# Performance work log

Hardware: AMD Instinct MI355X
Metric: run time of the kernel (lower is better)

Reference implementation:

```python
import jax, jax.numpy as jnp
import numpy as np

DIMS = [2048, 2048, 2048, 2048, 1000]
BATCH = 1024
N_RELAX = 25
RELAX_LR = 0.3
N_LAYERS = len(DIMS) - 1  # 4 weight matrices, states indexed 0..4


def setup_inputs() -> dict:
    key = jax.random.key(0)
    ks = jax.random.split(key, N_LAYERS + 1)
    inp = {"x": jax.random.normal(ks[0], (BATCH, DIMS[0]), jnp.float32)}
    for i in range(N_LAYERS):
        scale = np.float32(np.sqrt(2.0 / DIMS[i]))
        inp[f"W{i}"] = jax.random.normal(ks[i + 1], (DIMS[i], DIMS[i + 1]), jnp.float32) * scale
    # biases[0] is never used in forward; biases[1..4] init to zeros as in torch code
    for l in range(1, N_LAYERS + 1):
        inp[f"b{l}"] = jnp.zeros((DIMS[l],), jnp.float32)
    return inp


def _rho(t):
    return jnp.clip(t, 0.0, 1.0)


def _relax(x, Ws, bs):
    # bs[l-1] corresponds to original biases[l] (state l's bias), l = 1..N_LAYERS
    # feedforward initialization pass
    states = [x]
    h = x
    for l in range(N_LAYERS):
        h = _rho(h @ Ws[l] + bs[l])
        states.append(h)

    # Gauss-Seidel sweep: states[l-1] already updated this iteration when l uses it
    def sweep(carry, _):
        full = [x] + list(carry)
        for l in range(1, N_LAYERS + 1):
            ds = -full[l] + bs[l - 1] + _rho(full[l - 1]) @ Ws[l - 1]
            if l < N_LAYERS:
                ds = ds + _rho(full[l + 1]) @ Ws[l].T
            full[l] = _rho(full[l] + RELAX_LR * ds)
        return tuple(full[1:]), None

    carry, _ = jax.lax.scan(sweep, tuple(states[1:]), None, length=N_RELAX)
    return carry


def reference(x, W0, W1, W2, W3, b1, b2, b3, b4):
    Ws = [W0, W1, W2, W3]
    bs = [b1, b2, b3, b4]
    states = _relax(x, Ws, bs)
    return states[-1]  # [BATCH, DIMS[-1]]
```

## Files before the change

kernel.cpp:

```cpp
#include <hip/hip_runtime.h>
#include <hip/hip_bf16.h>

typedef _Float16 fp16_t;
typedef _Float16 v8h __attribute__((ext_vector_type(8)));
typedef float    v4f __attribute__((ext_vector_type(4)));

#define RELAX_LR 0.3f

__device__ __forceinline__ void async_cp16(const void* g, void* l) {
    __builtin_amdgcn_global_load_lds(
        (const __attribute__((address_space(1))) void*)g,
        (__attribute__((address_space(3))) void*)l, 16, 0, 0);
}

struct GJob {
    const fp16_t *A1, *B1t, *A2, *B2t;
    fp16_t* part;
    int K1, K2s, CK, Ntot;
};

__global__ __launch_bounds__(256, 2) void gemm_splitk_kernel(GJob j0, GJob j1, int nb0)
{
    __shared__ __align__(16) fp16_t As[2][2][128][32];
    __shared__ __align__(16) fp16_t Bs[2][2][128][32];

    const int tid  = threadIdx.x;
    const int lane = tid & 63;
    const int w    = tid >> 6;
    const int wm   = w >> 1;
    const int wn   = w & 1;
    const int quad = lane >> 4;
    const int lrow = lane & 15;

    int bblk = blockIdx.x;
    const GJob j = (bblk < nb0) ? j0 : j1;
    if (bblk >= nb0) bblk -= nb0;

    const int low3 = bblk & 7;
    const int g    = bblk >> 3;
    const int bm   = g & 7;
    const int c    = (g >> 3) * 8 + low3;
    int bn, z;
    if (j.Ntot == 2048) { bn = c >> 2; z = c & 3; }
    else                { bn = c >> 3; z = c & 7; }
    const int k0 = z * j.CK;

    const int sr = lane >> 2;
    const int sc = (lane & 3) * 8;
    const size_t rowA = (size_t)(bm * 128 + 32 * w + sr);
    const size_t rowB = (size_t)(bn * 128 + 32 * w + sr);
    const fp16_t* a1 = j.A1  + rowA * j.K1 + sc;
    const fp16_t* b1 = j.B1t + rowB * j.K1 + sc;
    const fp16_t* a2 = j.A2  ? j.A2  + rowA * j.K2s + sc : nullptr;
    const fp16_t* b2 = j.B2t ? j.B2t + rowB * j.K2s + sc : nullptr;
    const size_t s16a = (size_t)16 * j.K1;
    const size_t s16b = (size_t)16 * j.K2s;

    auto stage = [&](int buf, int kc) {
        const fp16_t *a0, *b0; size_t st;
        if (kc < j.K1) { a0 = a1 + kc;          b0 = b1 + kc;          st = s16a; }
        else           { a0 = a2 + (kc - j.K1); b0 = b2 + (kc - j.K1); st = s16b; }
        async_cp16(a0,           &As[buf][0][32 * w     ][0]);
        async_cp16(a0 + st,      &As[buf][0][32 * w + 16][0]);
        async_cp16(a0 + 32,      &As[buf][1][32 * w     ][0]);
        async_cp16(a0 + 32 + st, &As[buf][1][32 * w + 16][0]);
        async_cp16(b0,           &Bs[buf][0][32 * w     ][0]);
        async_cp16(b0 + st,      &Bs[buf][0][32 * w + 16][0]);
        async_cp16(b0 + 32,      &Bs[buf][1][32 * w     ][0]);
        async_cp16(b0 + 32 + st, &Bs[buf][1][32 * w + 16][0]);
    };

    v4f acc[4][4] = {};
    const int iters = j.CK >> 6;

    stage(0, k0);

    for (int it = 0; it < iters; ++it) {
        __syncthreads();
        if (it + 1 < iters) stage((it + 1) & 1, k0 + (it + 1) * 64);
        const int cur = it & 1;
        #pragma unroll
        for (int h = 0; h < 2; ++h) {
            v8h af[4], bv[4];
            #pragma unroll
            for (int fm = 0; fm < 4; ++fm)
                af[fm] = *(const v8h*)&As[cur][h][wm * 64 + fm * 16 + lrow][quad * 8];
            #pragma unroll
            for (int fn = 0; fn < 4; ++fn)
                bv[fn] = *(const v8h*)&Bs[cur][h][wn * 64 + fn * 16 + lrow][quad * 8];
            #pragma unroll
            for (int fm = 0; fm < 4; ++fm)
                #pragma unroll
                for (int fn = 0; fn < 4; ++fn)
                    acc[fm][fn] = __builtin_amdgcn_mfma_f32_16x16x32_f16(
                        af[fm], bv[fn], acc[fm][fn], 0, 0, 0);
        }
    }

    fp16_t* po = j.part + (size_t)z * 1024 * j.Ntot;
    const int rowbase = bm * 128 + wm * 64 + quad * 4;
    const int colbase = bn * 128 + wn * 64;
    #pragma unroll
    for (int fn = 0; fn < 4; ++fn) {
        const int col = colbase + fn * 16 + lrow;
        #pragma unroll
        for (int fm = 0; fm < 4; ++fm) {
            const int row = rowbase + fm * 16;
            #pragma unroll
            for (int r = 0; r < 4; ++r)
                po[(size_t)(row + r) * j.Ntot + col] = (fp16_t)acc[fm][fn][r];
        }
    }
}

struct RJob {
    const fp16_t* part;
    const float* bias;
    const float* extra;
    const fp16_t* s_old;
    fp16_t* outb;
    float* finout;
    int nz, Ntot, do_update;
};

__global__ __launch_bounds__(256) void reduce_update_kernel(RJob j0, RJob j1, int nb0)
{
    int b = blockIdx.x;
    const RJob j = (b < nb0) ? j0 : j1;
    if (b >= nb0) b -= nb0;
    const size_t e = ((size_t)b * 256 + threadIdx.x) * 8;

    float v[8];
    {
        const v8h p0 = *(const v8h*)(j.part + e);
        #pragma unroll
        for (int k = 0; k < 8; ++k) v[k] = (float)p0[k];
    }
    for (int z = 1; z < j.nz; ++z) {
        const v8h p = *(const v8h*)(j.part + (size_t)z * 1024 * j.Ntot + e);
        #pragma unroll
        for (int k = 0; k < 8; ++k) v[k] += (float)p[k];
    }
    const int col = (int)e & (j.Ntot - 1);
    if (j.extra) {
        const float4 e0 = *(const float4*)(j.extra + e);
        const float4 e1 = *(const float4*)(j.extra + e + 4);
        v[0] += e0.x; v[1] += e0.y; v[2] += e0.z; v[3] += e0.w;
        v[4] += e1.x; v[5] += e1.y; v[6] += e1.z; v[7] += e1.w;
    } else {
        const float4 b0 = *(const float4*)(j.bias + col);
        const float4 b1 = *(const float4*)(j.bias + col + 4);
        v[0] += b0.x; v[1] += b0.y; v[2] += b0.z; v[3] += b0.w;
        v[4] += b1.x; v[5] += b1.y; v[6] += b1.z; v[7] += b1.w;
    }
    if (j.do_update) {
        const v8h so = *(const v8h*)(j.s_old + e);
        #pragma unroll
        for (int k = 0; k < 8; ++k) {
            const float s = (float)so[k];
            v[k] = s + RELAX_LR * (v[k] - s);
        }
    }
    #pragma unroll
    for (int k = 0; k < 8; ++k) v[k] = fminf(fmaxf(v[k], 0.f), 1.f);
    v8h h;
    #pragma unroll
    for (int k = 0; k < 8; ++k) h[k] = (fp16_t)v[k];
    *(v8h*)(j.outb + e) = h;

    if (j.finout && col < 1000) {
        const int row = (int)(e >> 10);
        float* o = j.finout + (size_t)row * 1000 + col;
        float4 o0 = {v[0], v[1], v[2], v[3]};
        float4 o1 = {v[4], v[5], v[6], v[7]};
        *(float4*)o       = o0;
        *(float4*)(o + 4) = o1;
    }
}

__global__ __launch_bounds__(256) void makec1_kernel(
    const fp16_t* __restrict__ part, const float* __restrict__ bias,
    float* __restrict__ c1f, int total8)
{
    const int i = blockIdx.x * 256 + threadIdx.x;
    if (i >= total8) return;
    const size_t e = (size_t)i * 8;
    float v[8];
    {
        const v8h p0 = *(const v8h*)(part + e);
        #pragma unroll
        for (int k = 0; k < 8; ++k) v[k] = (float)p0[k];
    }
    #pragma unroll
    for (int z = 1; z < 4; ++z) {
        const v8h p = *(const v8h*)(part + (size_t)z * 1024 * 2048 + e);
        #pragma unroll
        for (int k = 0; k < 8; ++k) v[k] += (float)p[k];
    }
    const int col = (int)e & 2047;
    const float4 b0 = *(const float4*)(bias + col);
    const float4 b1 = *(const float4*)(bias + col + 4);
    v[0] += b0.x; v[1] += b0.y; v[2] += b0.z; v[3] += b0.w;
    v[4] += b1.x; v[5] += b1.y; v[6] += b1.z; v[7] += b1.w;
    float4 o0 = {v[0], v[1], v[2], v[3]};
    float4 o1 = {v[4], v[5], v[6], v[7]};
    *(float4*)(c1f + e)     = o0;
    *(float4*)(c1f + e + 4) = o1;
}

__global__ void conv_w_kernel(const float* __restrict__ W, int R, int C,
                              fp16_t* Wb, fp16_t* __restrict__ WbT,
                              int Rp, int Cp)
{
    __shared__ float t[32][33];
    const int tx = threadIdx.x & 31;
    const int ty = threadIdx.x >> 5;
    const int r0 = blockIdx.y * 32;
    const int c0 = blockIdx.x * 32;
    #pragma unroll
    for (int i = 0; i < 4; ++i) {
        const int r = r0 + ty + i * 8;
        const int c = c0 + tx;
        float v = 0.f;
        if (r < R && c < C) v = W[(size_t)r * C + c];
        t[ty + i * 8][tx] = v;
    }
    __syncthreads();
    if (Wb) {
        #pragma unroll
        for (int i = 0; i < 4; ++i) {
            const int r = r0 + ty + i * 8;
            const int c = c0 + tx;
            if (r < Rp && c < Cp) Wb[(size_t)r * Cp + c] = (fp16_t)t[ty + i * 8][tx];
        }
    }
    #pragma unroll
    for (int i = 0; i < 4; ++i) {
        const int cc = c0 + ty + i * 8;
        const int rr = r0 + tx;
        if (cc < Cp && rr < Rp) WbT[(size_t)cc * Rp + rr] = (fp16_t)t[tx][ty + i * 8];
    }
}

__global__ void conv_x_kernel(const float* __restrict__ x,
                              fp16_t* __restrict__ xb, fp16_t* __restrict__ rxb, int n)
{
    const int i = blockIdx.x * blockDim.x + threadIdx.x;
    if (i < n) {
        const float v = x[i];
        xb[i]  = (fp16_t)v;
        rxb[i] = (fp16_t)fminf(fmaxf(v, 0.f), 1.f);
    }
}

__global__ void pad_b4_kernel(const float* __restrict__ b4, float* __restrict__ b4p)
{
    const int i = blockIdx.x * blockDim.x + threadIdx.x;
    if (i < 1024) b4p[i] = (i < 1000) ? b4[i] : 0.f;
}

extern "C" void kernel_launch(void* const* d_in, const int* in_sizes, int n_in,
                              void* d_out, int out_size, void* d_ws, size_t ws_size,
                              hipStream_t stream)
{
    const float* x  = (const float*)d_in[0];
    const float* W0 = (const float*)d_in[1];
    const float* W1 = (const float*)d_in[2];
    const float* W2 = (const float*)d_in[3];
    const float* W3 = (const float*)d_in[4];
    const float* b1 = (const float*)d_in[5];
    const float* b2 = (const float*)d_in[6];
    const float* b3 = (const float*)d_in[7];
    const float* b4 = (const float*)d_in[8];
    float* out = (float*)d_out;

    char* p = (char*)d_ws;
    auto alloc = [&](size_t bytes) {
        char* q = p;
        p += (bytes + 255) & ~(size_t)255;
        return q;
    };

    fp16_t* xb    = (fp16_t*)alloc((size_t)1024 * 2048 * 2);
    fp16_t* rxb   = (fp16_t*)alloc((size_t)1024 * 2048 * 2);
    fp16_t* Wb1   = (fp16_t*)alloc((size_t)2048 * 2048 * 2);
    fp16_t* Wb2   = (fp16_t*)alloc((size_t)2048 * 2048 * 2);
    fp16_t* Wb3   = (fp16_t*)alloc((size_t)2048 * 1024 * 2);
    fp16_t* WbT0  = (fp16_t*)alloc((size_t)2048 * 2048 * 2);
    fp16_t* WbT1  = (fp16_t*)alloc((size_t)2048 * 2048 * 2);
    fp16_t* WbT2  = (fp16_t*)alloc((size_t)2048 * 2048 * 2);
    fp16_t* WbT3  = (fp16_t*)alloc((size_t)1024 * 2048 * 2);
    fp16_t* s1b   = (fp16_t*)alloc((size_t)1024 * 2048 * 2);
    fp16_t* s2b   = (fp16_t*)alloc((size_t)1024 * 2048 * 2);
    fp16_t* s3b   = (fp16_t*)alloc((size_t)1024 * 2048 * 2);
    fp16_t* s4b   = (fp16_t*)alloc((size_t)1024 * 1024 * 2);
    float*  b4p   = (float*)alloc(1024 * 4);
    float*  c1f   = (float*)alloc((size_t)1024 * 2048 * 4);
    fp16_t* partA = (fp16_t*)alloc((size_t)8 * 1024 * 1024 * 2);
    fp16_t* partB = (fp16_t*)alloc((size_t)4 * 1024 * 2048 * 2);
    (void)ws_size; (void)in_sizes; (void)n_in; (void)out_size;

    conv_x_kernel<<<(1024 * 2048 + 255) / 256, 256, 0, stream>>>(x, xb, rxb, 1024 * 2048);
    pad_b4_kernel<<<4, 256, 0, stream>>>(b4, b4p);
    conv_w_kernel<<<dim3(64, 64), 256, 0, stream>>>(W0, 2048, 2048, nullptr, WbT0, 2048, 2048);
    conv_w_kernel<<<dim3(64, 64), 256, 0, stream>>>(W1, 2048, 2048, Wb1, WbT1, 2048, 2048);
    conv_w_kernel<<<dim3(64, 64), 256, 0, stream>>>(W2, 2048, 2048, Wb2, WbT2, 2048, 2048);
    conv_w_kernel<<<dim3(32, 64), 256, 0, stream>>>(W3, 2048, 1000, Wb3, WbT3, 2048, 1024);

    const dim3 blk(256);
    const int rg2048 = 1024 * 2048 / 8 / 256;
    const int rg1024 = 1024 * 1024 / 8 / 256;

    const GJob jC1 = { rxb, WbT0, nullptr, nullptr, partA, 2048, 0,    512,  2048 };
    const GJob jI1 = { xb,  WbT0, nullptr, nullptr, partB, 2048, 0,    512,  2048 };
    const GJob jI2 = { s1b, WbT1, nullptr, nullptr, partB, 2048, 0,    512,  2048 };
    const GJob jI3 = { s2b, WbT2, nullptr, nullptr, partB, 2048, 0,    512,  2048 };
    const GJob jI4 = { s3b, WbT3, nullptr, nullptr, partA, 2048, 0,    256,  1024 };
    const GJob jL1 = { s2b, Wb1,  nullptr, nullptr, partB, 2048, 0,    512,  2048 };
    const GJob jL2 = { s1b, WbT1, s3b, Wb2,         partB, 2048, 2048, 1024, 2048 };
    const GJob jL3 = { s2b, WbT2, s4b, Wb3,         partB, 2048, 1024, 768,  2048 };
    const GJob jL4 = { s3b, WbT3, nullptr, nullptr, partA, 2048, 0,    256,  1024 };

    const RJob rI1 = { partB, b1,  nullptr, nullptr, s1b, nullptr, 4, 2048, 0 };
    const RJob rI2 = { partB, b2,  nullptr, nullptr, s2b, nullptr, 4, 2048, 0 };
    const RJob rI3 = { partB, b3,  nullptr, nullptr, s3b, nullptr, 4, 2048, 0 };
    const RJob rI4 = { partA, b4p, nullptr, nullptr, s4b, nullptr, 8, 1024, 0 };
    const RJob rL1 = { partB, nullptr, c1f, s1b, s1b, nullptr, 4, 2048, 1 };
    const RJob rL2 = { partB, b2,  nullptr, s2b, s2b, nullptr, 4, 2048, 1 };
    const RJob rL3 = { partB, b3,  nullptr, s3b, s3b, nullptr, 4, 2048, 1 };
    const RJob rL4 = { partA, b4p, nullptr, s4b, s4b, nullptr, 8, 1024, 1 };
    RJob rL4f = rL4; rL4f.finout = out;

    gemm_splitk_kernel<<<512, blk, 0, stream>>>(jC1, jC1, 512);
    makec1_kernel<<<rg2048, blk, 0, stream>>>(partA, b1, c1f, 1024 * 2048 / 8);

    gemm_splitk_kernel<<<512, blk, 0, stream>>>(jI1, jI1, 512);
    reduce_update_kernel<<<rg2048, blk, 0, stream>>>(rI1, rI1, rg2048);
    gemm_splitk_kernel<<<512, blk, 0, stream>>>(jI2, jI2, 512);
    reduce_update_kernel<<<rg2048, blk, 0, stream>>>(rI2, rI2, rg2048);
    gemm_splitk_kernel<<<512, blk, 0, stream>>>(jI3, jI3, 512);
    reduce_update_kernel<<<rg2048, blk, 0, stream>>>(rI3, rI3, rg2048);
    gemm_splitk_kernel<<<512, blk, 0, stream>>>(jI4, jI4, 512);
    reduce_update_kernel<<<rg1024, blk, 0, stream>>>(rI4, rI4, rg1024);

    gemm_splitk_kernel<<<512, blk, 0, stream>>>(jL1, jL1, 512);
    reduce_update_kernel<<<rg2048, blk, 0, stream>>>(rL1, rL1, rg2048);
    for (int it = 0; it < 25; ++it) {
        gemm_splitk_kernel<<<512, blk, 0, stream>>>(jL2, jL2, 512);
        reduce_update_kernel<<<rg2048, blk, 0, stream>>>(rL2, rL2, rg2048);
        gemm_splitk_kernel<<<512, blk, 0, stream>>>(jL3, jL3, 512);
        reduce_update_kernel<<<rg2048, blk, 0, stream>>>(rL3, rL3, rg2048);
        if (it < 24) {
            gemm_splitk_kernel<<<1024, blk, 0, stream>>>(jL4, jL1, 512);
            reduce_update_kernel<<<rg1024 + rg2048, blk, 0, stream>>>(rL4, rL1, rg1024);
        } else {
            gemm_splitk_kernel<<<512, blk, 0, stream>>>(jL4, jL4, 512);
            reduce_update_kernel<<<rg1024, blk, 0, stream>>>(rL4f, rL4f, rg1024);
        }
    }
}
```

Before: 2.411 ms.

## Fuse split-K reduction and state update into GEMM via intra-block K split

Replaces the global split-K GEMM plus separate reduce/update kernels with one fused kernel. Each block computes a 64x64 output tile, its four waves take disjoint K quarters with per-wave LDS double buffering, and the partials are reduced through LDS. Bias, extra term, relaxation update, clamp and the fp16/fp32 stores then happen in the epilogue. This removes the fp16 partial-sum round trips through global memory and halves kernel launches. In exchange the tiles are smaller, per-wave loads are synchronised with manual waitcnt, and the epilogue writes are scalar per element.

Result: slower. 3.226 ms (+33.8%).

```diff
diff --git a/kernel.cpp b/kernel.cpp
--- a/kernel.cpp
+++ b/kernel.cpp
@@ -1,5 +1,4 @@
 #include <hip/hip_runtime.h>
-#include <hip/hip_bf16.h>
 
 typedef _Float16 fp16_t;
 typedef _Float16 v8h __attribute__((ext_vector_type(8)));
@@ -13,199 +12,126 @@
         (__attribute__((address_space(3))) void*)l, 16, 0, 0);
 }
 
-struct GJob {
+struct FJob {
     const fp16_t *A1, *B1t, *A2, *B2t;
-    fp16_t* part;
-    int K1, K2s, CK, Ntot;
+    const float  *bias;
+    const float  *extra;
+    const fp16_t *s_old;
+    fp16_t       *outb;
+    float        *f32out;
+    float        *finout;
+    int K1, K2s, Ktot, Ntot;
 };
 
-__global__ __launch_bounds__(256, 2) void gemm_splitk_kernel(GJob j0, GJob j1, int nb0)
-{
-    __shared__ __align__(16) fp16_t As[2][2][128][32];
-    __shared__ __align__(16) fp16_t Bs[2][2][128][32];
+__global__ __launch_bounds__(256, 2) void gemm_fused_kernel(FJob j0, FJob j1, int nb0)
+{
+    __shared__ __align__(16) fp16_t sm[4][2][2][64][32];
 
     const int tid  = threadIdx.x;
     const int lane = tid & 63;
     const int w    = tid >> 6;
-    const int wm   = w >> 1;
-    const int wn   = w & 1;
     const int quad = lane >> 4;
     const int lrow = lane & 15;
 
     int bblk = blockIdx.x;
-    const GJob j = (bblk < nb0) ? j0 : j1;
+    const FJob j = (bblk < nb0) ? j0 : j1;
     if (bblk >= nb0) bblk -= nb0;
 
-    const int low3 = bblk & 7;
-    const int g    = bblk >> 3;
-    const int bm   = g & 7;
-    const int c    = (g >> 3) * 8 + low3;
-    int bn, z;
-    if (j.Ntot == 2048) { bn = c >> 2; z = c & 3; }
-    else                { bn = c >> 3; z = c & 7; }
-    const int k0 = z * j.CK;
-
-    const int sr = lane >> 2;
-    const int sc = (lane & 3) * 8;
-    const size_t rowA = (size_t)(bm * 128 + 32 * w + sr);
-    const size_t rowB = (size_t)(bn * 128 + 32 * w + sr);
-    const fp16_t* a1 = j.A1  + rowA * j.K1 + sc;
-    const fp16_t* b1 = j.B1t + rowB * j.K1 + sc;
-    const fp16_t* a2 = j.A2  ? j.A2  + rowA * j.K2s + sc : nullptr;
-    const fp16_t* b2 = j.B2t ? j.B2t + rowB * j.K2s + sc : nullptr;
-    const size_t s16a = (size_t)16 * j.K1;
-    const size_t s16b = (size_t)16 * j.K2s;
+    const int xcd = bblk & 7;
+    const int g   = bblk >> 3;
+    const int bm  = g & 15;
+    const int bn  = (j.Ntot == 2048) ? xcd * 4 + (g >> 4)
+                                     : xcd * 2 + (g >> 4);
+
+    const int KQ  = j.Ktot >> 2;
+    const int kq0 = w * KQ;
+
+    const int sr  = lane >> 2;
+    const int sc8 = (lane & 3) * 8;
+    const fp16_t* a1 = j.A1  + (size_t)(bm * 64 + sr) * j.K1 + sc8;
+    const fp16_t* b1 = j.B1t + (size_t)(bn * 64 + sr) * j.K1 + sc8;
+    const fp16_t* a2 = j.A2  ? j.A2  + (size_t)(bm * 64 + sr) * j.K2s + sc8 : nullptr;
+    const fp16_t* b2 = j.B2t ? j.B2t + (size_t)(bn * 64 + sr) * j.K2s + sc8 : nullptr;
 
     auto stage = [&](int buf, int kc) {
-        const fp16_t *a0, *b0; size_t st;
-        if (kc < j.K1) { a0 = a1 + kc;          b0 = b1 + kc;          st = s16a; }
-        else           { a0 = a2 + (kc - j.K1); b0 = b2 + (kc - j.K1); st = s16b; }
-        async_cp16(a0,           &As[buf][0][32 * w     ][0]);
-        async_cp16(a0 + st,      &As[buf][0][32 * w + 16][0]);
-        async_cp16(a0 + 32,      &As[buf][1][32 * w     ][0]);
-        async_cp16(a0 + 32 + st, &As[buf][1][32 * w + 16][0]);
-        async_cp16(b0,           &Bs[buf][0][32 * w     ][0]);
-        async_cp16(b0 + st,      &Bs[buf][0][32 * w + 16][0]);
-        async_cp16(b0 + 32,      &Bs[buf][1][32 * w     ][0]);
-        async_cp16(b0 + 32 + st, &Bs[buf][1][32 * w + 16][0]);
+        const fp16_t *as, *bs; size_t st;
+        if (kc < j.K1) { as = a1 + kc;          bs = b1 + kc;          st = (size_t)16 * j.K1;  }
+        else           { as = a2 + (kc - j.K1); bs = b2 + (kc - j.K1); st = (size_t)16 * j.K2s; }
+        #pragma unroll
+        for (int ch = 0; ch < 4; ++ch) {
+            async_cp16(as + (size_t)ch * st, &sm[w][buf][0][ch * 16][0]);
+            async_cp16(bs + (size_t)ch * st, &sm[w][buf][1][ch * 16][0]);
+        }
     };
 
     v4f acc[4][4] = {};
-    const int iters = j.CK >> 6;
-
-    stage(0, k0);
-
+    const int iters = KQ >> 5;
+
+    stage(0, kq0);
     for (int it = 0; it < iters; ++it) {
-        __syncthreads();
-        if (it + 1 < iters) stage((it + 1) & 1, k0 + (it + 1) * 64);
         const int cur = it & 1;
-        #pragma unroll
-        for (int h = 0; h < 2; ++h) {
-            v8h af[4], bv[4];
-            #pragma unroll
-            for (int fm = 0; fm < 4; ++fm)
-                af[fm] = *(const v8h*)&As[cur][h][wm * 64 + fm * 16 + lrow][quad * 8];
+        if (it + 1 < iters) {
+            asm volatile("s_waitcnt lgkmcnt(0)" ::: "memory");
+            stage(cur ^ 1, kq0 + (it + 1) * 32);
+            asm volatile("s_waitcnt vmcnt(8)" ::: "memory");
+        } else {
+            asm volatile("s_waitcnt vmcnt(0)" ::: "memory");
+        }
+        v8h af[4], bv[4];
+        #pragma unroll
+        for (int fm = 0; fm < 4; ++fm)
+            af[fm] = *(const v8h*)&sm[w][cur][0][fm * 16 + lrow][quad * 8];
+        #pragma unroll
+        for (int fn = 0; fn < 4; ++fn)
+            bv[fn] = *(const v8h*)&sm[w][cur][1][fn * 16 + lrow][quad * 8];
+        __builtin_amdgcn_s_setprio(1);
+        #pragma unroll
+        for (int fm = 0; fm < 4; ++fm)
             #pragma unroll
             for (int fn = 0; fn < 4; ++fn)
-                bv[fn] = *(const v8h*)&Bs[cur][h][wn * 64 + fn * 16 + lrow][quad * 8];
-            #pragma unroll
-            for (int fm = 0; fm < 4; ++fm)
-                #pragma unroll
-                for (int fn = 0; fn < 4; ++fn)
-                    acc[fm][fn] = __builtin_amdgcn_mfma_f32_16x16x32_f16(
-                        af[fm], bv[fn], acc[fm][fn], 0, 0, 0);
-        }
-    }
-
-    fp16_t* po = j.part + (size_t)z * 1024 * j.Ntot;
-    const int rowbase = bm * 128 + wm * 64 + quad * 4;
-    const int colbase = bn * 128 + wn * 64;
-    #pragma unroll
-    for (int fn = 0; fn < 4; ++fn) {
-        const int col = colbase + fn * 16 + lrow;
-        #pragma unroll
-        for (int fm = 0; fm < 4; ++fm) {
-            const int row = rowbase + fm * 16;
+                acc[fm][fn] = __builtin_amdgcn_mfma_f32_16x16x32_f16(
+                    af[fm], bv[fn], acc[fm][fn], 0, 0, 0);
+        __builtin_amdgcn_s_setprio(0);
+    }
+
+    __syncthreads();
+    float* red = (float*)sm;
+    #pragma unroll
+    for (int fm = 0; fm < 4; ++fm)
+        #pragma unroll
+        for (int fn = 0; fn < 4; ++fn)
             #pragma unroll
             for (int r = 0; r < 4; ++r)
-                po[(size_t)(row + r) * j.Ntot + col] = (fp16_t)acc[fm][fn][r];
-        }
-    }
-}
-
-struct RJob {
-    const fp16_t* part;
-    const float* bias;
-    const float* extra;
-    const fp16_t* s_old;
-    fp16_t* outb;
-    float* finout;
-    int nz, Ntot, do_update;
-};
-
-__global__ __launch_bounds__(256) void reduce_update_kernel(RJob j0, RJob j1, int nb0)
-{
-    int b = blockIdx.x;
-    const RJob j = (b < nb0) ? j0 : j1;
-    if (b >= nb0) b -= nb0;
-    const size_t e = ((size_t)b * 256 + threadIdx.x) * 8;
-
-    float v[8];
-    {
-        const v8h p0 = *(const v8h*)(j.part + e);
-        #pragma unroll
-        for (int k = 0; k < 8; ++k) v[k] = (float)p0[k];
-    }
-    for (int z = 1; z < j.nz; ++z) {
-        const v8h p = *(const v8h*)(j.part + (size_t)z * 1024 * j.Ntot + e);
-        #pragma unroll
-        for (int k = 0; k < 8; ++k) v[k] += (float)p[k];
-    }
-    const int col = (int)e & (j.Ntot - 1);
-    if (j.extra) {
-        const float4 e0 = *(const float4*)(j.extra + e);
-        const float4 e1 = *(const float4*)(j.extra + e + 4);
-        v[0] += e0.x; v[1] += e0.y; v[2] += e0.z; v[3] += e0.w;
-        v[4] += e1.x; v[5] += e1.y; v[6] += e1.z; v[7] += e1.w;
-    } else {
-        const float4 b0 = *(const float4*)(j.bias + col);
-        const float4 b1 = *(const float4*)(j.bias + col + 4);
-        v[0] += b0.x; v[1] += b0.y; v[2] += b0.z; v[3] += b0.w;
-        v[4] += b1.x; v[5] += b1.y; v[6] += b1.z; v[7] += b1.w;
-    }
-    if (j.do_update) {
-        const v8h so = *(const v8h*)(j.s_old + e);
-        #pragma unroll
-        for (int k = 0; k < 8; ++k) {
-            const float s = (float)so[k];
-            v[k] = s + RELAX_LR * (v[k] - s);
-        }
-    }
-    #pragma unroll
-    for (int k = 0; k < 8; ++k) v[k] = fminf(fmaxf(v[k], 0.f), 1.f);
-    v8h h;
-    #pragma unroll
-    for (int k = 0; k < 8; ++k) h[k] = (fp16_t)v[k];
-    *(v8h*)(j.outb + e) = h;
-
-    if (j.finout && col < 1000) {
-        const int row = (int)(e >> 10);
-        float* o = j.finout + (size_t)row * 1000 + col;
-        float4 o0 = {v[0], v[1], v[2], v[3]};
-        float4 o1 = {v[4], v[5], v[6], v[7]};
-        *(float4*)o       = o0;
-        *(float4*)(o + 4) = o1;
-    }
-}
-
-__global__ __launch_bounds__(256) void makec1_kernel(
-    const fp16_t* __restrict__ part, const float* __restrict__ bias,
-    float* __restrict__ c1f, int total8)
-{
-    const int i = blockIdx.x * 256 + threadIdx.x;
-    if (i >= total8) return;
-    const size_t e = (size_t)i * 8;
-    float v[8];
-    {
-        const v8h p0 = *(const v8h*)(part + e);
-        #pragma unroll
-        for (int k = 0; k < 8; ++k) v[k] = (float)p0[k];
-    }
-    #pragma unroll
-    for (int z = 1; z < 4; ++z) {
-        const v8h p = *(const v8h*)(part + (size_t)z * 1024 * 2048 + e);
-        #pragma unroll
-        for (int k = 0; k < 8; ++k) v[k] += (float)p[k];
-    }
-    const int col = (int)e & 2047;
-    const float4 b0 = *(const float4*)(bias + col);
-    const float4 b1 = *(const float4*)(bias + col + 4);
-    v[0] += b0.x; v[1] += b0.y; v[2] += b0.z; v[3] += b0.w;
-    v[4] += b1.x; v[5] += b1.y; v[6] += b1.z; v[7] += b1.w;
-    float4 o0 = {v[0], v[1], v[2], v[3]};
-    float4 o1 = {v[4], v[5], v[6], v[7]};
-    *(float4*)(c1f + e)     = o0;
-    *(float4*)(c1f + e + 4) = o1;
+                red[((w * 64 + fm * 16 + fn * 4 + r) << 6) + lane] = acc[fm][fn][r];
+    __syncthreads();
+
+    const int rowbase = bm * 64 + w * 16 + quad * 4;
+    const int colbase = bn * 64;
+    #pragma unroll
+    for (int u = 0; u < 16; ++u) {
+        const int s = w * 16 + u;
+        float v = red[( s        << 6) + lane]
+                + red[((64  + s) << 6) + lane]
+                + red[((128 + s) << 6) + lane]
+                + red[((192 + s) << 6) + lane];
+        const int row = rowbase + (u & 3);
+        const int col = colbase + (u >> 2) * 16 + lrow;
+        const size_t idx = (size_t)row * j.Ntot + col;
+        if (j.extra) v += j.extra[idx];
+        else         v += j.bias[col];
+        if (j.s_old) {
+            const float so = (float)j.s_old[idx];
+            v = so + RELAX_LR * (v - so);
+        }
+        if (j.f32out) {
+            j.f32out[idx] = v;
+        } else {
+            v = fminf(fmaxf(v, 0.f), 1.f);
+            j.outb[idx] = (fp16_t)v;
+            if (j.finout && col < 1000)
+                j.finout[(size_t)row * 1000 + col] = v;
+        }
+    }
 }
 
 __global__ void conv_w_kernel(const float* __restrict__ W, int R, int C,
@@ -296,8 +222,6 @@
     fp16_t* s4b   = (fp16_t*)alloc((size_t)1024 * 1024 * 2);
     float*  b4p   = (float*)alloc(1024 * 4);
     float*  c1f   = (float*)alloc((size_t)1024 * 2048 * 4);
-    fp16_t* partA = (fp16_t*)alloc((size_t)8 * 1024 * 1024 * 2);
-    fp16_t* partB = (fp16_t*)alloc((size_t)4 * 1024 * 2048 * 2);
     (void)ws_size; (void)in_sizes; (void)n_in; (void)out_size;
 
     conv_x_kernel<<<(1024 * 2048 + 255) / 256, 256, 0, stream>>>(x, xb, rxb, 1024 * 2048);
@@ -308,54 +232,33 @@
     conv_w_kernel<<<dim3(32, 64), 256, 0, stream>>>(W3, 2048, 1000, Wb3, WbT3, 2048, 1024);
 
     const dim3 blk(256);
-    const int rg2048 = 1024 * 2048 / 8 / 256;
-    const int rg1024 = 1024 * 1024 / 8 / 256;
-
-    const GJob jC1 = { rxb, WbT0, nullptr, nullptr, partA, 2048, 0,    512,  2048 };
-    const GJob jI1 = { xb,  WbT0, nullptr, nullptr, partB, 2048, 0,    512,  2048 };
-    const GJob jI2 = { s1b, WbT1, nullptr, nullptr, partB, 2048, 0,    512,  2048 };
-    const GJob jI3 = { s2b, WbT2, nullptr, nullptr, partB, 2048, 0,    512,  2048 };
-    const GJob jI4 = { s3b, WbT3, nullptr, nullptr, partA, 2048, 0,    256,  1024 };
-    const GJob jL1 = { s2b, Wb1,  nullptr, nullptr, partB, 2048, 0,    512,  2048 };
-    const GJob jL2 = { s1b, WbT1, s3b, Wb2,         partB, 2048, 2048, 1024, 2048 };
-    const GJob jL3 = { s2b, WbT2, s4b, Wb3,         partB, 2048, 1024, 768,  2048 };
-    const GJob jL4 = { s3b, WbT3, nullptr, nullptr, partA, 2048, 0,    256,  1024 };
-
-    const RJob rI1 = { partB, b1,  nullptr, nullptr, s1b, nullptr, 4, 2048, 0 };
-    const RJob rI2 = { partB, b2,  nullptr, nullptr, s2b, nullptr, 4, 2048, 0 };
-    const RJob rI3 = { partB, b3,  nullptr, nullptr, s3b, nullptr, 4, 2048, 0 };
-    const RJob rI4 = { partA, b4p, nullptr, nullptr, s4b, nullptr, 8, 1024, 0 };
-    const RJob rL1 = { partB, nullptr, c1f, s1b, s1b, nullptr, 4, 2048, 1 };
-    const RJob rL2 = { partB, b2,  nullptr, s2b, s2b, nullptr, 4, 2048, 1 };
-    const RJob rL3 = { partB, b3,  nullptr, s3b, s3b, nullptr, 4, 2048, 1 };
-    const RJob rL4 = { partA, b4p, nullptr, s4b, s4b, nullptr, 8, 1024, 1 };
-    RJob rL4f = rL4; rL4f.finout = out;
-
-    gemm_splitk_kernel<<<512, blk, 0, stream>>>(jC1, jC1, 512);
-    makec1_kernel<<<rg2048, blk, 0, stream>>>(partA, b1, c1f, 1024 * 2048 / 8);
-
-    gemm_splitk_kernel<<<512, blk, 0, stream>>>(jI1, jI1, 512);
-    reduce_update_kernel<<<rg2048, blk, 0, stream>>>(rI1, rI1, rg2048);
-    gemm_splitk_kernel<<<512, blk, 0, stream>>>(jI2, jI2, 512);
-    reduce_update_kernel<<<rg2048, blk, 0, stream>>>(rI2, rI2, rg2048);
-    gemm_splitk_kernel<<<512, blk, 0, stream>>>(jI3, jI3, 512);
-    reduce_update_kernel<<<rg2048, blk, 0, stream>>>(rI3, rI3, rg2048);
-    gemm_splitk_kernel<<<512, blk, 0, stream>>>(jI4, jI4, 512);
-    reduce_update_kernel<<<rg1024, blk, 0, stream>>>(rI4, rI4, rg1024);
-
-    gemm_splitk_kernel<<<512, blk, 0, stream>>>(jL1, jL1, 512);
-    reduce_update_kernel<<<rg2048, blk, 0, stream>>>(rL1, rL1, rg2048);
+
+    const FJob jC1 = { rxb, WbT0, nullptr, nullptr, b1,  nullptr, nullptr, nullptr, c1f,  nullptr, 2048, 0,    2048, 2048 };
+    const FJob jI1 = { xb,  WbT0, nullptr, nullptr, b1,  nullptr, nullptr, s1b, nullptr, nullptr, 2048, 0,    2048, 2048 };
+    const FJob jI2 = { s1b, WbT1, nullptr, nullptr, b2,  nullptr, nullptr, s2b, nullptr, nullptr, 2048, 0,    2048, 2048 };
+    const FJob jI3 = { s2b, WbT2, nullptr, nullptr, b3,  nullptr, nullptr, s3b, nullptr, nullptr, 2048, 0,    2048, 2048 };
+    const FJob jI4 = { s3b, WbT3, nullptr, nullptr, b4p, nullptr, nullptr, s4b, nullptr, nullptr, 2048, 0,    2048, 1024 };
+    const FJob jL1 = { s2b, Wb1,  nullptr, nullptr, nullptr, c1f, s1b,     s1b, nullptr, nullptr, 2048, 0,    2048, 2048 };
+    const FJob jL2 = { s1b, WbT1, s3b, Wb2,         b2,  nullptr, s2b,     s2b, nullptr, nullptr, 2048, 2048, 4096, 2048 };
+    const FJob jL3 = { s2b, WbT2, s4b, Wb3,         b3,  nullptr, s3b,     s3b, nullptr, nullptr, 2048, 1024, 3072, 2048 };
+    const FJob jL4 = { s3b, WbT3, nullptr, nullptr, b4p, nullptr, s4b,     s4b, nullptr, nullptr, 2048, 0,    2048, 1024 };
+    FJob jL4f = jL4; jL4f.finout = out;
+
+    gemm_fused_kernel<<<512, blk, 0, stream>>>(jC1, jC1, 512);
+
+    gemm_fused_kernel<<<512, blk, 0, stream>>>(jI1, jI1, 512);
+    gemm_fused_kernel<<<512, blk, 0, stream>>>(jI2, jI2, 512);
+    gemm_fused_kernel<<<512, blk, 0, stream>>>(jI3, jI3, 512);
+    gemm_fused_kernel<<<256, blk, 0, stream>>>(jI4, jI4, 256);
+
+    gemm_fused_kernel<<<512, blk, 0, stream>>>(jL1, jL1, 512);
     for (int it = 0; it < 25; ++it) {
-        gemm_splitk_kernel<<<512, blk, 0, stream>>>(jL2, jL2, 512);
-        reduce_update_kernel<<<rg2048, blk, 0, stream>>>(rL2, rL2, rg2048);
-        gemm_splitk_kernel<<<512, blk, 0, stream>>>(jL3, jL3, 512);
-        reduce_update_kernel<<<rg2048, blk, 0, stream>>>(rL3, rL3, rg2048);
+        gemm_fused_kernel<<<512, blk, 0, stream>>>(jL2, jL2, 512);
+        gemm_fused_kernel<<<512, blk, 0, stream>>>(jL3, jL3, 512);
         if (it < 24) {
-            gemm_splitk_kernel<<<1024, blk, 0, stream>>>(jL4, jL1, 512);
-            reduce_update_kernel<<<rg1024 + rg2048, blk, 0, stream>>>(rL4, rL1, rg1024);
+            gemm_fused_kernel<<<768, blk, 0, stream>>>(jL4, jL1, 256);
         } else {
-            gemm_splitk_kernel<<<512, blk, 0, stream>>>(jL4, jL4, 512);
-            reduce_update_kernel<<<rg1024, blk, 0, stream>>>(rL4f, rL4f, rg1024);
-        }
-    }
-}
+            gemm_fused_kernel<<<256, blk, 0, stream>>>(jL4f, jL4f, 256);
+        }
+    }
+}
```

## Halve GEMM K-tile and use split-K 8 for N=2048 GEMMs

Applied to the files above, without the earlier changes.

Shrinks the per-stage K tile from 64 to 32, which halves shared memory per block, and raises launch bounds to 4 blocks per CU. All 2048-wide GEMMs move from 4-way to 8-way split-K, doubling grid sizes to give more blocks for the GPU's CUs. The reduce kernels and makec1 now sum 8 partials, which doubles the fp16 partial buffer and the reduction memory traffic. Each iteration also does fewer MFMAs per barrier, so synchronisation overhead is relatively higher.

Result: slower. 2.650 ms (+9.9%).

```diff
diff --git a/kernel.cpp b/kernel.cpp
--- a/kernel.cpp
+++ b/kernel.cpp
@@ -1,5 +1,4 @@
 #include <hip/hip_runtime.h>
-#include <hip/hip_bf16.h>
 
 typedef _Float16 fp16_t;
 typedef _Float16 v8h __attribute__((ext_vector_type(8)));
@@ -19,10 +18,10 @@
     int K1, K2s, CK, Ntot;
 };
 
-__global__ __launch_bounds__(256, 2) void gemm_splitk_kernel(GJob j0, GJob j1, int nb0)
-{
-    __shared__ __align__(16) fp16_t As[2][2][128][32];
-    __shared__ __align__(16) fp16_t Bs[2][2][128][32];
+__global__ __launch_bounds__(256, 4) void gemm_splitk_kernel(GJob j0, GJob j1, int nb0)
+{
+    __shared__ __align__(16) fp16_t As[2][128][32];
+    __shared__ __align__(16) fp16_t Bs[2][128][32];
 
     const int tid  = threadIdx.x;
     const int lane = tid & 63;
@@ -40,10 +39,9 @@
     const int g    = bblk >> 3;
     const int bm   = g & 7;
     const int c    = (g >> 3) * 8 + low3;
-    int bn, z;
-    if (j.Ntot == 2048) { bn = c >> 2; z = c & 3; }
-    else                { bn = c >> 3; z = c & 7; }
-    const int k0 = z * j.CK;
+    const int bn   = c >> 3;
+    const int z    = c & 7;
+    const int k0   = z * j.CK;
 
     const int sr = lane >> 2;
     const int sc = (lane & 3) * 8;
@@ -60,41 +58,34 @@
         const fp16_t *a0, *b0; size_t st;
         if (kc < j.K1) { a0 = a1 + kc;          b0 = b1 + kc;          st = s16a; }
         else           { a0 = a2 + (kc - j.K1); b0 = b2 + (kc - j.K1); st = s16b; }
-        async_cp16(a0,           &As[buf][0][32 * w     ][0]);
-        async_cp16(a0 + st,      &As[buf][0][32 * w + 16][0]);
-        async_cp16(a0 + 32,      &As[buf][1][32 * w     ][0]);
-        async_cp16(a0 + 32 + st, &As[buf][1][32 * w + 16][0]);
-        async_cp16(b0,           &Bs[buf][0][32 * w     ][0]);
-        async_cp16(b0 + st,      &Bs[buf][0][32 * w + 16][0]);
-        async_cp16(b0 + 32,      &Bs[buf][1][32 * w     ][0]);
-        async_cp16(b0 + 32 + st, &Bs[buf][1][32 * w + 16][0]);
+        async_cp16(a0,      &As[buf][32 * w     ][0]);
+        async_cp16(a0 + st, &As[buf][32 * w + 16][0]);
+        async_cp16(b0,      &Bs[buf][32 * w     ][0]);
+        async_cp16(b0 + st, &Bs[buf][32 * w + 16][0]);
     };
 
     v4f acc[4][4] = {};
-    const int iters = j.CK >> 6;
+    const int iters = j.CK >> 5;
 
     stage(0, k0);
 
     for (int it = 0; it < iters; ++it) {
         __syncthreads();
-        if (it + 1 < iters) stage((it + 1) & 1, k0 + (it + 1) * 64);
+        if (it + 1 < iters) stage((it + 1) & 1, k0 + (it + 1) * 32);
         const int cur = it & 1;
-        #pragma unroll
-        for (int h = 0; h < 2; ++h) {
-            v8h af[4], bv[4];
-            #pragma unroll
-            for (int fm = 0; fm < 4; ++fm)
-                af[fm] = *(const v8h*)&As[cur][h][wm * 64 + fm * 16 + lrow][quad * 8];
+        v8h af[4], bv[4];
+        #pragma unroll
+        for (int fm = 0; fm < 4; ++fm)
+            af[fm] = *(const v8h*)&As[cur][wm * 64 + fm * 16 + lrow][quad * 8];
+        #pragma unroll
+        for (int fn = 0; fn < 4; ++fn)
+            bv[fn] = *(const v8h*)&Bs[cur][wn * 64 + fn * 16 + lrow][quad * 8];
+        #pragma unroll
+        for (int fm = 0; fm < 4; ++fm)
             #pragma unroll
             for (int fn = 0; fn < 4; ++fn)
-                bv[fn] = *(const v8h*)&Bs[cur][h][wn * 64 + fn * 16 + lrow][quad * 8];
-            #pragma unroll
-            for (int fm = 0; fm < 4; ++fm)
-                #pragma unroll
-                for (int fn = 0; fn < 4; ++fn)
-                    acc[fm][fn] = __builtin_amdgcn_mfma_f32_16x16x32_f16(
-                        af[fm], bv[fn], acc[fm][fn], 0, 0, 0);
-        }
+                acc[fm][fn] = __builtin_amdgcn_mfma_f32_16x16x32_f16(
+                    af[fm], bv[fn], acc[fm][fn], 0, 0, 0);
     }
 
     fp16_t* po = j.part + (size_t)z * 1024 * j.Ntot;
@@ -192,7 +183,7 @@
         for (int k = 0; k < 8; ++k) v[k] = (float)p0[k];
     }
     #pragma unroll
-    for (int z = 1; z < 4; ++z) {
+    for (int z = 1; z < 8; ++z) {
         const v8h p = *(const v8h*)(part + (size_t)z * 1024 * 2048 + e);
         #pragma unroll
         for (int k = 0; k < 8; ++k) v[k] += (float)p[k];
@@ -297,7 +288,7 @@
     float*  b4p   = (float*)alloc(1024 * 4);
     float*  c1f   = (float*)alloc((size_t)1024 * 2048 * 4);
     fp16_t* partA = (fp16_t*)alloc((size_t)8 * 1024 * 1024 * 2);
-    fp16_t* partB = (fp16_t*)alloc((size_t)4 * 1024 * 2048 * 2);
+    fp16_t* partB = (fp16_t*)alloc((size_t)8 * 1024 * 2048 * 2);
     (void)ws_size; (void)in_sizes; (void)n_in; (void)out_size;
 
     conv_x_kernel<<<(1024 * 2048 + 255) / 256, 256, 0, stream>>>(x, xb, rxb, 1024 * 2048);
@@ -311,47 +302,47 @@
     const int rg2048 = 1024 * 2048 / 8 / 256;
     const int rg1024 = 1024 * 1024 / 8 / 256;
 
-    const GJob jC1 = { rxb, WbT0, nullptr, nullptr, partA, 2048, 0,    512,  2048 };
-    const GJob jI1 = { xb,  WbT0, nullptr, nullptr, partB, 2048, 0,    512,  2048 };
-    const GJob jI2 = { s1b, WbT1, nullptr, nullptr, partB, 2048, 0,    512,  2048 };
-    const GJob jI3 = { s2b, WbT2, nullptr, nullptr, partB, 2048, 0,    512,  2048 };
-    const GJob jI4 = { s3b, WbT3, nullptr, nullptr, partA, 2048, 0,    256,  1024 };
-    const GJob jL1 = { s2b, Wb1,  nullptr, nullptr, partB, 2048, 0,    512,  2048 };
-    const GJob jL2 = { s1b, WbT1, s3b, Wb2,         partB, 2048, 2048, 1024, 2048 };
-    const GJob jL3 = { s2b, WbT2, s4b, Wb3,         partB, 2048, 1024, 768,  2048 };
-    const GJob jL4 = { s3b, WbT3, nullptr, nullptr, partA, 2048, 0,    256,  1024 };
-
-    const RJob rI1 = { partB, b1,  nullptr, nullptr, s1b, nullptr, 4, 2048, 0 };
-    const RJob rI2 = { partB, b2,  nullptr, nullptr, s2b, nullptr, 4, 2048, 0 };
-    const RJob rI3 = { partB, b3,  nullptr, nullptr, s3b, nullptr, 4, 2048, 0 };
+    const GJob jC1 = { rxb, WbT0, nullptr, nullptr, partB, 2048, 0,    256, 2048 };
+    const GJob jI1 = { xb,  WbT0, nullptr, nullptr, partB, 2048, 0,    256, 2048 };
+    const GJob jI2 = { s1b, WbT1, nullptr, nullptr, partB, 2048, 0,    256, 2048 };
+    const GJob jI3 = { s2b, WbT2, nullptr, nullptr, partB, 2048, 0,    256, 2048 };
+    const GJob jI4 = { s3b, WbT3, nullptr, nullptr, partA, 2048, 0,    256, 1024 };
+    const GJob jL1 = { s2b, Wb1,  nullptr, nullptr, partB, 2048, 0,    256, 2048 };
+    const GJob jL2 = { s1b, WbT1, s3b, Wb2,         partB, 2048, 2048, 512, 2048 };
+    const GJob jL3 = { s2b, WbT2, s4b, Wb3,         partB, 2048, 1024, 384, 2048 };
+    const GJob jL4 = { s3b, WbT3, nullptr, nullptr, partA, 2048, 0,    256, 1024 };
+
+    const RJob rI1 = { partB, b1,  nullptr, nullptr, s1b, nullptr, 8, 2048, 0 };
+    const RJob rI2 = { partB, b2,  nullptr, nullptr, s2b, nullptr, 8, 2048, 0 };
+    const RJob rI3 = { partB, b3,  nullptr, nullptr, s3b, nullptr, 8, 2048, 0 };
     const RJob rI4 = { partA, b4p, nullptr, nullptr, s4b, nullptr, 8, 1024, 0 };
-    const RJob rL1 = { partB, nullptr, c1f, s1b, s1b, nullptr, 4, 2048, 1 };
-    const RJob rL2 = { partB, b2,  nullptr, s2b, s2b, nullptr, 4, 2048, 1 };
-    const RJob rL3 = { partB, b3,  nullptr, s3b, s3b, nullptr, 4, 2048, 1 };
+    const RJob rL1 = { partB, nullptr, c1f, s1b, s1b, nullptr, 8, 2048, 1 };
+    const RJob rL2 = { partB, b2,  nullptr, s2b, s2b, nullptr, 8, 2048, 1 };
+    const RJob rL3 = { partB, b3,  nullptr, s3b, s3b, nullptr, 8, 2048, 1 };
     const RJob rL4 = { partA, b4p, nullptr, s4b, s4b, nullptr, 8, 1024, 1 };
     RJob rL4f = rL4; rL4f.finout = out;
 
-    gemm_splitk_kernel<<<512, blk, 0, stream>>>(jC1, jC1, 512);
-    makec1_kernel<<<rg2048, blk, 0, stream>>>(partA, b1, c1f, 1024 * 2048 / 8);
-
-    gemm_splitk_kernel<<<512, blk, 0, stream>>>(jI1, jI1, 512);
+    gemm_splitk_kernel<<<1024, blk, 0, stream>>>(jC1, jC1, 1024);
+    makec1_kernel<<<rg2048, blk, 0, stream>>>(partB, b1, c1f, 1024 * 2048 / 8);
+
+    gemm_splitk_kernel<<<1024, blk, 0, stream>>>(jI1, jI1, 1024);
     reduce_update_kernel<<<rg2048, blk, 0, stream>>>(rI1, rI1, rg2048);
-    gemm_splitk_kernel<<<512, blk, 0, stream>>>(jI2, jI2, 512);
+    gemm_splitk_kernel<<<1024, blk, 0, stream>>>(jI2, jI2, 1024);
     reduce_update_kernel<<<rg2048, blk, 0, stream>>>(rI2, rI2, rg2048);
-    gemm_splitk_kernel<<<512, blk, 0, stream>>>(jI3, jI3, 512);
+    gemm_splitk_kernel<<<1024, blk, 0, stream>>>(jI3, jI3, 1024);
     reduce_update_kernel<<<rg2048, blk, 0, stream>>>(rI3, rI3, rg2048);
     gemm_splitk_kernel<<<512, blk, 0, stream>>>(jI4, jI4, 512);
     reduce_update_kernel<<<rg1024, blk, 0, stream>>>(rI4, rI4, rg1024);
 
-    gemm_splitk_kernel<<<512, blk, 0, stream>>>(jL1, jL1, 512);
+    gemm_splitk_kernel<<<1024, blk, 0, stream>>>(jL1, jL1, 1024);
     reduce_update_kernel<<<rg2048, blk, 0, stream>>>(rL1, rL1, rg2048);
     for (int it = 0; it < 25; ++it) {
-        gemm_splitk_kernel<<<512, blk, 0, stream>>>(jL2, jL2, 512);
+        gemm_splitk_kernel<<<1024, blk, 0, stream>>>(jL2, jL2, 1024);
         reduce_update_kernel<<<rg2048, blk, 0, stream>>>(rL2, rL2, rg2048);
-        gemm_splitk_kernel<<<512, blk, 0, stream>>>(jL3, jL3, 512);
+        gemm_splitk_kernel<<<1024, blk, 0, stream>>>(jL3, jL3, 1024);
         reduce_update_kernel<<<rg2048, blk, 0, stream>>>(rL3, rL3, rg2048);
         if (it < 24) {
-            gemm_splitk_kernel<<<1024, blk, 0, stream>>>(jL4, jL1, 512);
+            gemm_splitk_kernel<<<1536, blk, 0, stream>>>(jL4, jL1, 512);
             reduce_update_kernel<<<rg1024 + rg2048, blk, 0, stream>>>(rL4, rL1, rg1024);
         } else {
             gemm_splitk_kernel<<<512, blk, 0, stream>>>(jL4, jL4, 512);
```

## Switch GEMM to 32x32x16 MFMA with XOR-swizzled LDS layout

Applied to the files above, without the earlier changes.

Replaces the 4x4 grid of 16x16x32 MFMA tiles per wave with a 2x2 grid of 32x32x16 MFMA tiles, so fewer LDS fragment loads feed the same amount of math. It also XOR-swizzles the 16-byte column chunk when staging A and B into shared memory and when reading them back, to avoid LDS bank conflicts on the new access pattern. The epilogue is rewritten for the 32x32 accumulator layout. The partial-sum stores stay strided fp16 scalar writes.

After: 2.610 ms. +8.3%, slower.

```diff
diff --git a/kernel.cpp b/kernel.cpp
--- a/kernel.cpp
+++ b/kernel.cpp
@@ -1,9 +1,8 @@
 #include <hip/hip_runtime.h>
-#include <hip/hip_bf16.h>
 
 typedef _Float16 fp16_t;
-typedef _Float16 v8h __attribute__((ext_vector_type(8)));
-typedef float    v4f __attribute__((ext_vector_type(4)));
+typedef _Float16 v8h  __attribute__((ext_vector_type(8)));
+typedef float    v16f __attribute__((ext_vector_type(16)));
 
 #define RELAX_LR 0.3f
 
@@ -29,24 +28,24 @@
     const int w    = tid >> 6;
     const int wm   = w >> 1;
     const int wn   = w & 1;
-    const int quad = lane >> 4;
-    const int lrow = lane & 15;
+    const int l31  = lane & 31;
+    const int g    = lane >> 5;
 
     int bblk = blockIdx.x;
     const GJob j = (bblk < nb0) ? j0 : j1;
     if (bblk >= nb0) bblk -= nb0;
 
     const int low3 = bblk & 7;
-    const int g    = bblk >> 3;
-    const int bm   = g & 7;
-    const int c    = (g >> 3) * 8 + low3;
+    const int gg   = bblk >> 3;
+    const int bm   = gg & 7;
+    const int c    = (gg >> 3) * 8 + low3;
     int bn, z;
     if (j.Ntot == 2048) { bn = c >> 2; z = c & 3; }
     else                { bn = c >> 3; z = c & 7; }
     const int k0 = z * j.CK;
 
     const int sr = lane >> 2;
-    const int sc = (lane & 3) * 8;
+    const int sc = (((lane & 3) ^ (sr & 3))) * 8;
     const size_t rowA = (size_t)(bm * 128 + 32 * w + sr);
     const size_t rowB = (size_t)(bn * 128 + 32 * w + sr);
     const fp16_t* a1 = j.A1  + rowA * j.K1 + sc;
@@ -70,7 +69,7 @@
         async_cp16(b0 + 32 + st, &Bs[buf][1][32 * w + 16][0]);
     };
 
-    v4f acc[4][4] = {};
+    v16f acc[2][2] = {};
     const int iters = j.CK >> 6;
 
     stage(0, k0);
@@ -80,37 +79,34 @@
         if (it + 1 < iters) stage((it + 1) & 1, k0 + (it + 1) * 64);
         const int cur = it & 1;
         #pragma unroll
-        for (int h = 0; h < 2; ++h) {
-            v8h af[4], bv[4];
+        for (int s = 0; s < 4; ++s) {
+            const int h  = s >> 1;
+            const int cs = ((((s & 1) * 2 + g) ^ (l31 & 3))) * 8;
+            const v8h a0v = *(const v8h*)&As[cur][h][wm * 64      + l31][cs];
+            const v8h a1v = *(const v8h*)&As[cur][h][wm * 64 + 32 + l31][cs];
+            const v8h b0v = *(const v8h*)&Bs[cur][h][wn * 64      + l31][cs];
+            const v8h b1v = *(const v8h*)&Bs[cur][h][wn * 64 + 32 + l31][cs];
+            acc[0][0] = __builtin_amdgcn_mfma_f32_32x32x16_f16(a0v, b0v, acc[0][0], 0, 0, 0);
+            acc[0][1] = __builtin_amdgcn_mfma_f32_32x32x16_f16(a0v, b1v, acc[0][1], 0, 0, 0);
+            acc[1][0] = __builtin_amdgcn_mfma_f32_32x32x16_f16(a1v, b0v, acc[1][0], 0, 0, 0);
+            acc[1][1] = __builtin_amdgcn_mfma_f32_32x32x16_f16(a1v, b1v, acc[1][1], 0, 0, 0);
+        }
+    }
+
+    fp16_t* po = j.part + (size_t)z * 1024 * j.Ntot;
+    const int rowb = bm * 128 + wm * 64 + g * 4;
+    const int colb = bn * 128 + wn * 64 + l31;
+    #pragma unroll
+    for (int fm2 = 0; fm2 < 2; ++fm2)
+        #pragma unroll
+        for (int fn2 = 0; fn2 < 2; ++fn2) {
+            const int col = colb + fn2 * 32;
             #pragma unroll
-            for (int fm = 0; fm < 4; ++fm)
-                af[fm] = *(const v8h*)&As[cur][h][wm * 64 + fm * 16 + lrow][quad * 8];
-            #pragma unroll
-            for (int fn = 0; fn < 4; ++fn)
-                bv[fn] = *(const v8h*)&Bs[cur][h][wn * 64 + fn * 16 + lrow][quad * 8];
-            #pragma unroll
-            for (int fm = 0; fm < 4; ++fm)
-                #pragma unroll
-                for (int fn = 0; fn < 4; ++fn)
-                    acc[fm][fn] = __builtin_amdgcn_mfma_f32_16x16x32_f16(
-                        af[fm], bv[fn], acc[fm][fn], 0, 0, 0);
-        }
-    }
-
-    fp16_t* po = j.part + (size_t)z * 1024 * j.Ntot;
-    const int rowbase = bm * 128 + wm * 64 + quad * 4;
-    const int colbase = bn * 128 + wn * 64;
-    #pragma unroll
-    for (int fn = 0; fn < 4; ++fn) {
-        const int col = colbase + fn * 16 + lrow;
-        #pragma unroll
-        for (int fm = 0; fm < 4; ++fm) {
-            const int row = rowbase + fm * 16;
-            #pragma unroll
-            for (int r = 0; r < 4; ++r)
-                po[(size_t)(row + r) * j.Ntot + col] = (fp16_t)acc[fm][fn][r];
-        }
-    }
+            for (int r = 0; r < 16; ++r) {
+                const int row = rowb + fm2 * 32 + (r & 3) + 8 * (r >> 2);
+                po[(size_t)row * j.Ntot + col] = (fp16_t)acc[fm2][fn2][r];
+            }
+        }
 }
 
 struct RJob {
```
